# Performance work log

Hardware: AMD Instinct MI355X
Metric: run time of the kernel (lower is better)

## Reference

```python
import jax, jax.numpy as jnp
import numpy as np

C_S, C_Z, C_H, H, PQ, PV = 384, 128, 16, 12, 4, 8
B, N = 1, 512
OUT_DIM = H * (C_H + PV * 4 + C_Z)  # 2112


def setup_inputs() -> dict:
    key = jax.random.key(0)
    ks = jax.random.split(key, 20)
    std = 0.02
    def lin(k, fan_in, fan_out):
        k1, k2 = jax.random.split(k)
        w = jax.random.normal(k1, (fan_in, fan_out), jnp.float32) * std
        b = jax.random.normal(k2, (fan_out,), jnp.float32) * std
        return w, b
    wq, bq = lin(ks[0], C_S, H * C_H)
    wk, bk = lin(ks[1], C_S, H * C_H)
    wv, bv = lin(ks[2], C_S, H * C_H)
    wqp, bqp = lin(ks[3], C_S, H * PQ * 3)
    wkp, bkp = lin(ks[4], C_S, H * PQ * 3)
    wvp, bvp = lin(ks[5], C_S, H * PV * 3)
    wb, bb = lin(ks[6], C_Z, H)
    wo, bo = lin(ks[7], OUT_DIM, C_S)
    return {
        "s": jax.random.normal(ks[8], (B, N, C_S), jnp.float32),
        "z": jax.random.normal(ks[9], (B, N, N, C_Z), jnp.float32),
        "translations": jax.random.normal(ks[10], (B, N, 3), jnp.float32),
        "rotations": jax.random.normal(ks[11], (B, N, 3, 3), jnp.float32),
        "mask": jnp.ones((B, N), jnp.int32),
        "wq": wq, "bq": bq, "wk": wk, "bk": bk, "wv": wv, "bv": bv,
        "wqp": wqp, "bqp": bqp, "wkp": wkp, "bkp": bkp, "wvp": wvp, "bvp": bvp,
        "wb": wb, "bb": bb, "wo": wo, "bo": bo,
    }


def reference(s, z, translations, rotations, mask,
              wq, bq, wk, bk, wv, bv, wqp, bqp, wkp, bkp, wvp, bvp,
              wb, bb, wo, bo):
    b_, n_ = s.shape[0], s.shape[1]
    # scalar q/k/v: (B,N,H,C)
    q = (s @ wq + bq).reshape(b_, n_, H, C_H)
    k = (s @ wk + bk).reshape(b_, n_, H, C_H)
    v = (s @ wv + bv).reshape(b_, n_, H, C_H)
    # points: (B,N,H,P,3), moved to global frame
    qp = (s @ wqp + bqp).reshape(b_, n_, H, PQ, 3)
    kp = (s @ wkp + bkp).reshape(b_, n_, H, PQ, 3)
    t = translations[:, :, None, None, :]  # (B,N,1,1,3)
    qpg = jnp.einsum('bnij,bnhpj->bnhpi', rotations, qp) + t
    kpg = jnp.einsum('bnij,bnhpj->bnhpi', rotations, kp) + t
    # scalar attention: (B,N,M,H)
    attn_scalar = jnp.einsum('bnhc,bmhc->bnmh', q, k) / np.sqrt(C_H).astype(np.float32)
    # point-distance attention: (B,N,M,H)
    diff = qpg[:, :, None] - kpg[:, None]           # (B,N,M,H,P,3)
    attn_points = -0.5 * jnp.sum(diff * diff, axis=(-1, -2))
    # pair bias: (B,N,M,H)
    bias = z @ wb + bb
    attn = attn_scalar + attn_points + bias
    mask2d = (mask[:, None, :] * mask[:, :, None])[..., None]  # (B,N,M,1)
    attn = jnp.where(mask2d == 0, -jnp.inf, attn)
    w = jax.nn.softmax(attn, axis=2)  # over keys M
    # scalar values
    v_out_scalar = jnp.einsum('bnmh,bmhc->bnhc', w, v)
    # point values -> global -> attend -> back to local frame
    vp = (s @ wvp + bvp).reshape(b_, n_, H, PV, 3)
    vpg = jnp.einsum('bnij,bnhpj->bnhpi', rotations, vp) + t
    v_out_points = jnp.einsum('bnmh,bmhpi->bnhpi', w, vpg)
    rot_T = jnp.swapaxes(rotations, -2, -1)
    v_out_points_local = jnp.einsum('bnij,bnhpj->bnhpi', rot_T, v_out_points - t)
    v_out_points_flat = v_out_points_local.reshape(b_, n_, H, PV * 3)
    point_norms = jnp.linalg.norm(v_out_points_local, axis=-1)  # (B,N,H,P)
    # pair features
    pair_features = jnp.einsum('bnmh,bnmc->bnhc', w, z)
    features = jnp.concatenate(
        [v_out_scalar, v_out_points_flat, point_norms, pair_features], axis=-1
    ).reshape(b_, n_, -1)  # (B,N,OUT_DIM)
    return features @ wo + bo
```

## Files before the change

### kernel.cpp

```cpp
#include <hip/hip_runtime.h>

#define NN 512
#define CS 384
#define CZ 128
#define NH 12
#define PROJW 1152
#define FEAT 2112
#define OUTC 384
#define KC 12
#define KTILES 11

#define WPROJ 0
#define WFEAT 589824
#define WW    1671168
#define WOUTP 1671168
#define WKT   4816896

__global__ __launch_bounds__(256) void proj_gemm(
    const float* __restrict__ s,
    const float* __restrict__ wq, const float* __restrict__ bq,
    const float* __restrict__ wk, const float* __restrict__ bk,
    const float* __restrict__ wv, const float* __restrict__ bv,
    const float* __restrict__ wqp, const float* __restrict__ bqp,
    const float* __restrict__ wkp, const float* __restrict__ bkp,
    const float* __restrict__ wvp, const float* __restrict__ bvp,
    const float* __restrict__ rot, const float* __restrict__ trans,
    float* __restrict__ proj, float* __restrict__ kT)
{
    __shared__ float As[32*68];
    __shared__ float Ws[32*52];
    int tid = threadIdx.x;
    int gm0 = blockIdx.x * 64;
    int gc0 = blockIdx.y * 48;
    const float *w, *b; int ldw, lc0;
    if      (gc0 < 192) { w = wq;  b = bq;  ldw = 192; lc0 = gc0;       }
    else if (gc0 < 384) { w = wk;  b = bk;  ldw = 192; lc0 = gc0 - 192; }
    else if (gc0 < 576) { w = wv;  b = bv;  ldw = 192; lc0 = gc0 - 384; }
    else if (gc0 < 720) { w = wqp; b = bqp; ldw = 144; lc0 = gc0 - 576; }
    else if (gc0 < 864) { w = wkp; b = bkp; ldw = 144; lc0 = gc0 - 720; }
    else                { w = wvp; b = bvp; ldw = 288; lc0 = gc0 - 864; }

    int mi = tid >> 4, ni = tid & 15;
    int m0 = mi * 4, n0 = ni * 3;
    float acc[4][3] = {};

    for (int k0 = 0; k0 < CS; k0 += 32) {
        for (int idx = tid; idx < 2048; idx += 256) {
            int r = idx >> 5, c = idx & 31;
            As[c*68 + r] = s[(gm0 + r)*CS + k0 + c];
        }
        for (int idx = tid; idx < 1536; idx += 256) {
            int c = idx / 48, j = idx - c*48;
            Ws[c*52 + j] = w[(k0 + c)*ldw + lc0 + j];
        }
        __syncthreads();
        #pragma unroll 8
        for (int kk = 0; kk < 32; ++kk) {
            float4 a = *(const float4*)&As[kk*68 + m0];
            float w0 = Ws[kk*52 + n0], w1 = Ws[kk*52 + n0 + 1], w2 = Ws[kk*52 + n0 + 2];
            acc[0][0] += a.x*w0; acc[0][1] += a.x*w1; acc[0][2] += a.x*w2;
            acc[1][0] += a.y*w0; acc[1][1] += a.y*w1; acc[1][2] += a.y*w2;
            acc[2][0] += a.z*w0; acc[2][1] += a.z*w1; acc[2][2] += a.z*w2;
            acc[3][0] += a.w*w0; acc[3][1] += a.w*w1; acc[3][2] += a.w*w2;
        }
        __syncthreads();
    }

    float b0 = b[lc0 + n0], b1 = b[lc0 + n0 + 1], b2 = b[lc0 + n0 + 2];
    if (gc0 >= 576) {
        #pragma unroll
        for (int i = 0; i < 4; ++i) {
            int gm = gm0 + m0 + i;
            const float* R = rot + gm*9;
            const float* T = trans + gm*3;
            float x = acc[i][0] + b0, y = acc[i][1] + b1, zz = acc[i][2] + b2;
            float gx = R[0]*x + R[1]*y + R[2]*zz + T[0];
            float gy = R[3]*x + R[4]*y + R[5]*zz + T[1];
            float gz = R[6]*x + R[7]*y + R[8]*zz + T[2];
            float* dst = proj + (size_t)gm*PROJW + gc0 + n0;
            dst[0] = gx; dst[1] = gy; dst[2] = gz;
            if (gc0 >= 720 && gc0 < 864) {
                int c = 192 + (gc0 - 720) + n0;
                kT[(size_t)(c+0)*NN + gm] = gx;
                kT[(size_t)(c+1)*NN + gm] = gy;
                kT[(size_t)(c+2)*NN + gm] = gz;
            }
        }
    } else {
        #pragma unroll
        for (int i = 0; i < 4; ++i) {
            int gm = gm0 + m0 + i;
            float v0 = acc[i][0] + b0, v1 = acc[i][1] + b1, v2 = acc[i][2] + b2;
            float* dst = proj + (size_t)gm*PROJW + gc0 + n0;
            dst[0] = v0; dst[1] = v1; dst[2] = v2;
            if (gc0 >= 192 && gc0 < 384) {
                int c = gc0 - 192 + n0;
                kT[(size_t)(c+0)*NN + gm] = v0;
                kT[(size_t)(c+1)*NN + gm] = v1;
                kT[(size_t)(c+2)*NN + gm] = v2;
            }
        }
    }
}

__global__ __launch_bounds__(256) void bias_gemm(
    const float* __restrict__ z,
    const float* __restrict__ wb, const float* __restrict__ bb,
    float* __restrict__ ww)
{
    __shared__ float zl[64*128];
    __shared__ float sb[64*12];
    int tid = threadIdx.x;
    size_t r0 = (size_t)blockIdx.x * 64;

    const float4* src = (const float4*)(z + r0*CZ);
    float4 v[8];
    #pragma unroll
    for (int k = 0; k < 8; ++k) v[k] = src[tid + k*256];
    #pragma unroll
    for (int k = 0; k < 8; ++k) {
        int i = tid + k*256;
        int r = i >> 5, c4 = i & 31;
        *(float4*)&zl[r*128 + ((c4 ^ (r & 7)) << 2)] = v[k];
    }
    __syncthreads();

    int r = tid & 63, hg = tid >> 6;
    int h0 = __builtin_amdgcn_readfirstlane(hg * 3);
    const float* wbp = wb + h0;
    float a0 = bb[h0], a1 = bb[h0+1], a2 = bb[h0+2];
    #pragma unroll 8
    for (int c4 = 0; c4 < 32; ++c4) {
        float4 zv = *(const float4*)&zl[r*128 + ((c4 ^ (r & 7)) << 2)];
        int cb = c4*4;
        a0 += zv.x*wbp[cb*12]     + zv.y*wbp[(cb+1)*12]     + zv.z*wbp[(cb+2)*12]     + zv.w*wbp[(cb+3)*12];
        a1 += zv.x*wbp[cb*12 + 1] + zv.y*wbp[(cb+1)*12 + 1] + zv.z*wbp[(cb+2)*12 + 1] + zv.w*wbp[(cb+3)*12 + 1];
        a2 += zv.x*wbp[cb*12 + 2] + zv.y*wbp[(cb+1)*12 + 2] + zv.z*wbp[(cb+2)*12 + 2] + zv.w*wbp[(cb+3)*12 + 2];
    }
    float* sd = &sb[r*12 + h0];
    sd[0] = a0; sd[1] = a1; sd[2] = a2;
    __syncthreads();
    if (tid < 192) ((float4*)(ww + r0*12))[tid] = ((const float4*)sb)[tid];
}

__global__ __launch_bounds__(512, 4) void score_kernel(
    const float* __restrict__ proj, const float* __restrict__ kT,
    float* __restrict__ ww,
    const int* __restrict__ mask,
    const float* __restrict__ rot, const float* __restrict__ trans,
    float* __restrict__ feat)
{
    int n = blockIdx.x, tid = threadIdx.x;
    __shared__ float s_e[NN*12];
    __shared__ float s_q[336];
    __shared__ float s_pts[288];
    __shared__ float s_red[384];
    __shared__ float s_M[NH], s_S[NH];

    {
        const float4* src = (const float4*)(ww + (size_t)n*NN*12);
        float4* dst = (float4*)s_e;
        #pragma unroll
        for (int k = 0; k < 3; ++k) dst[tid + k*512] = src[tid + k*512];
    }
    if (tid < 336) s_q[tid] = proj[(size_t)n*PROJW + (tid < 192 ? tid : 384 + tid)];
    int mn = mask[n];
    __syncthreads();

    {
        int m = tid;
        bool ok = (mn != 0) && (mask[m] != 0);
        float sc[12];
        #pragma unroll 2
        for (int h = 0; h < NH; ++h) {
            const float* qh  = &s_q[h*16];
            const float* kTh = kT + (size_t)(h*16)*NN + m;
            float dot = 0.f;
            #pragma unroll
            for (int cc = 0; cc < 16; ++cc) dot += qh[cc] * kTh[(size_t)cc*NN];
            const float* qph  = &s_q[192 + h*12];
            const float* kpTh = kT + (size_t)(192 + h*12)*NN + m;
            float pts = 0.f;
            #pragma unroll
            for (int j = 0; j < 12; ++j) { float d = qph[j] - kpTh[(size_t)j*NN]; pts += d*d; }
            sc[h] = dot*0.25f - 0.5f*pts;
        }
        float* row = &s_e[m*12];
        #pragma unroll
        for (int h = 0; h < NH; ++h) {
            float v = sc[h] + row[h];
            row[h] = ok ? v : -1e30f;
        }
    }
    __syncthreads();
    if (tid < 384) {
        int i = tid / 12, h = tid - i*12;
        float mx = -1e30f;
        for (int mm = i*16; mm < i*16 + 16; ++mm) mx = fmaxf(mx, s_e[mm*12 + h]);
        s_red[tid] = mx;
    }
    __syncthreads();
    if (tid < NH) {
        float mx = -1e30f;
        #pragma unroll
        for (int i = 0; i < 32; ++i) mx = fmaxf(mx, s_red[i*12 + tid]);
        s_M[tid] = mx;
    }
    __syncthreads();
    {
        float M[12];
        #pragma unroll
        for (int h = 0; h < NH; ++h) M[h] = s_M[h];
        float* row = &s_e[tid*12];
        float4 a = *(float4*)row, b4 = *(float4*)(row+4), c4 = *(float4*)(row+8);
        a.x = __expf(a.x - M[0]);  a.y = __expf(a.y - M[1]);
        a.z = __expf(a.z - M[2]);  a.w = __expf(a.w - M[3]);
        b4.x = __expf(b4.x - M[4]); b4.y = __expf(b4.y - M[5]);
        b4.z = __expf(b4.z - M[6]); b4.w = __expf(b4.w - M[7]);
        c4.x = __expf(c4.x - M[8]); c4.y = __expf(c4.y - M[9]);
        c4.z = __expf(c4.z - M[10]); c4.w = __expf(c4.w - M[11]);
        *(float4*)row = a; *(float4*)(row+4) = b4; *(float4*)(row+8) = c4;
    }
    __syncthreads();
    if (tid < 384) {
        int i = tid / 12, h = tid - i*12;
        float sm = 0.f;
        for (int mm = i*16; mm < i*16 + 16; ++mm) sm += s_e[mm*12 + h];
        s_red[tid] = sm;
    }
    __syncthreads();
    if (tid < NH) {
        float sm = 0.f;
        #pragma unroll
        for (int i = 0; i < 32; ++i) sm += s_red[i*12 + tid];
        s_S[tid] = sm;
    }
    __syncthreads();
    {
        float iS[12];
        #pragma unroll
        for (int h = 0; h < NH; ++h) iS[h] = 1.0f / s_S[h];
        float* row = &s_e[tid*12];
        float4 a = *(float4*)row, b4 = *(float4*)(row+4), c4 = *(float4*)(row+8);
        a.x *= iS[0]; a.y *= iS[1]; a.z *= iS[2]; a.w *= iS[3];
        b4.x *= iS[4]; b4.y *= iS[5]; b4.z *= iS[6]; b4.w *= iS[7];
        c4.x *= iS[8]; c4.y *= iS[9]; c4.z *= iS[10]; c4.w *= iS[11];
        *(float4*)row = a; *(float4*)(row+4) = b4; *(float4*)(row+8) = c4;
    }
    __syncthreads();
    {
        float4* dst = (float4*)(ww + (size_t)n*NN*12);
        const float4* src = (const float4*)s_e;
        #pragma unroll
        for (int k = 0; k < 3; ++k) dst[tid + k*512] = src[tid + k*512];
    }

    float* fout = feat + (size_t)n * FEAT;

    {
        int o = tid;
        if (o < 480) {
            int col, h; bool isPt = (o >= 192);
            if (!isPt) { col = 384 + o;       h = o >> 4; }
            else       { int p = o - 192; col = 864 + p; h = p / 24; }
            const float* pc = proj + col;
            float acc0 = 0.f, acc1 = 0.f;
            #pragma unroll 8
            for (int mm = 0; mm < NN; mm += 2) {
                acc0 += s_e[(mm  )*12 + h] * pc[(size_t)(mm  )*PROJW];
                acc1 += s_e[(mm+1)*12 + h] * pc[(size_t)(mm+1)*PROJW];
            }
            float acc = acc0 + acc1;
            if (!isPt) fout[h*176 + (o & 15)] = acc;
            else       s_pts[o - 192] = acc;
        }
    }
    __syncthreads();
    if (tid < 96) {
        int h = tid >> 3, p = tid & 7;
        const float* R = rot + n*9;
        const float* T = trans + n*3;
        float x  = s_pts[h*24 + p*3]     - T[0];
        float y  = s_pts[h*24 + p*3 + 1] - T[1];
        float zz = s_pts[h*24 + p*3 + 2] - T[2];
        float lx = R[0]*x + R[3]*y + R[6]*zz;
        float ly = R[1]*x + R[4]*y + R[7]*zz;
        float lz = R[2]*x + R[5]*y + R[8]*zz;
        float* fo = fout + h*176 + 16;
        fo[p*3] = lx; fo[p*3+1] = ly; fo[p*3+2] = lz;
        fout[h*176 + 40 + p] = sqrtf(lx*lx + ly*ly + lz*lz);
    }
}

__global__ __launch_bounds__(512, 4) void pair_kernel(
    const float* __restrict__ ww, const float* __restrict__ z,
    float* __restrict__ feat)
{
    int n = blockIdx.x, tid = threadIdx.x;
    __shared__ float s_w[NN*12];
    __shared__ float s_p[4*NH*128];
    {
        const float4* src = (const float4*)(ww + (size_t)n*NN*12);
        float4* dst = (float4*)s_w;
        #pragma unroll
        for (int k = 0; k < 3; ++k) dst[tid + k*512] = src[tid + k*512];
    }
    __syncthreads();
    int c = tid & 127, mh = tid >> 7;
    const float* zb = z + ((size_t)n*NN + mh*128) * CZ + c;
    float pacc[12] = {};
    #pragma unroll 4
    for (int mm = 0; mm < 128; ++mm) {
        float zv = zb[(size_t)mm * CZ];
        const float* wr = &s_w[(mh*128 + mm)*12];
        float4 a = *(const float4*)wr, b4 = *(const float4*)(wr+4), c4 = *(const float4*)(wr+8);
        pacc[0] += a.x*zv;  pacc[1] += a.y*zv;  pacc[2] += a.z*zv;  pacc[3] += a.w*zv;
        pacc[4] += b4.x*zv; pacc[5] += b4.y*zv; pacc[6] += b4.z*zv; pacc[7] += b4.w*zv;
        pacc[8] += c4.x*zv; pacc[9] += c4.y*zv; pacc[10] += c4.z*zv; pacc[11] += c4.w*zv;
    }
    #pragma unroll
    for (int h = 0; h < NH; ++h) s_p[(mh*NH + h)*128 + c] = pacc[h];
    __syncthreads();
    {
        float* fout = feat + (size_t)n * FEAT;
        int cc = tid & 127, jh = tid >> 7;
        #pragma unroll
        for (int j = 0; j < 3; ++j) {
            int h = jh*3 + j;
            fout[h*176 + 48 + cc] = s_p[h*128 + cc] + s_p[(NH + h)*128 + cc]
                                  + s_p[(2*NH + h)*128 + cc] + s_p[(3*NH + h)*128 + cc];
        }
    }
}

__global__ __launch_bounds__(256) void out_gemm(
    const float* __restrict__ feat, const float* __restrict__ wo,
    float* __restrict__ pout)
{
    __shared__ float As[16*68];
    __shared__ float Ws[16*68];
    int tid = threadIdx.x;
    int gm0 = blockIdx.x * 64, gn0 = blockIdx.y * 64;
    int kc = blockIdx.z;
    int kbase = kc * (KTILES*16);
    int mi = tid >> 4, ni = tid & 15;
    int m0 = mi * 4, n0 = ni * 4;
    float acc[4][4] = {};

    int ar = tid >> 4, ac = tid & 15;
    int wr = tid >> 6, wc = tid & 63;

    float fa0, fa1, fa2, fa3, wa0, wa1, wa2, wa3;
    float fb0, fb1, fb2, fb3, wb0, wb1, wb2, wb3;
    {
        const float* fp = feat + (size_t)(gm0 + ar)*FEAT + kbase + ac;
        fa0 = fp[0]; fa1 = fp[16*FEAT]; fa2 = fp[32*FEAT]; fa3 = fp[48*FEAT];
        const float* wp = wo + (size_t)(kbase + wr)*OUTC + gn0 + wc;
        wa0 = wp[0]; wa1 = wp[4*OUTC]; wa2 = wp[8*OUTC]; wa3 = wp[12*OUTC];
    }
    for (int kt = 0; kt < KTILES; ++kt) {
        As[ac*68 + ar]      = fa0;
        As[ac*68 + ar + 16] = fa1;
        As[ac*68 + ar + 32] = fa2;
        As[ac*68 + ar + 48] = fa3;
        Ws[wr*68 + wc]        = wa0;
        Ws[(wr+4)*68 + wc]    = wa1;
        Ws[(wr+8)*68 + wc]    = wa2;
        Ws[(wr+12)*68 + wc]   = wa3;
        if (kt + 1 < KTILES) {
            int k0 = kbase + (kt+1)*16;
            const float* fp = feat + (size_t)(gm0 + ar)*FEAT + k0 + ac;
            fb0 = fp[0]; fb1 = fp[16*FEAT]; fb2 = fp[32*FEAT]; fb3 = fp[48*FEAT];
            const float* wp = wo + (size_t)(k0 + wr)*OUTC + gn0 + wc;
            wb0 = wp[0]; wb1 = wp[4*OUTC]; wb2 = wp[8*OUTC]; wb3 = wp[12*OUTC];
        }
        __syncthreads();
        #pragma unroll
        for (int kk = 0; kk < 16; ++kk) {
            float4 a = *(const float4*)&As[kk*68 + m0];
            float4 w = *(const float4*)&Ws[kk*68 + n0];
            acc[0][0] += a.x*w.x; acc[0][1] += a.x*w.y; acc[0][2] += a.x*w.z; acc[0][3] += a.x*w.w;
            acc[1][0] += a.y*w.x; acc[1][1] += a.y*w.y; acc[1][2] += a.y*w.z; acc[1][3] += a.y*w.w;
            acc[2][0] += a.z*w.x; acc[2][1] += a.z*w.y; acc[2][2] += a.z*w.z; acc[2][3] += a.z*w.w;
            acc[3][0] += a.w*w.x; acc[3][1] += a.w*w.y; acc[3][2] += a.w*w.z; acc[3][3] += a.w*w.w;
        }
        __syncthreads();
        fa0 = fb0; fa1 = fb1; fa2 = fb2; fa3 = fb3;
        wa0 = wb0; wa1 = wb1; wa2 = wb2; wa3 = wb3;
    }
    float* pb = pout + (size_t)kc * (NN*OUTC);
    #pragma unroll
    for (int i = 0; i < 4; ++i)
        *(float4*)&pb[(size_t)(gm0 + m0 + i)*OUTC + gn0 + n0] =
            make_float4(acc[i][0], acc[i][1], acc[i][2], acc[i][3]);
}

__global__ __launch_bounds__(256) void out_reduce(
    const float* __restrict__ pout, const float* __restrict__ bo,
    float* __restrict__ out)
{
    int idx4 = blockIdx.x * 256 + threadIdx.x;
    int col4 = idx4 % 96;
    const float4* b4 = (const float4*)bo;
    float4 acc = b4[col4];
    #pragma unroll
    for (int kc = 0; kc < KC; ++kc) {
        float4 p = ((const float4*)(pout + (size_t)kc*(NN*OUTC)))[idx4];
        acc.x += p.x; acc.y += p.y; acc.z += p.z; acc.w += p.w;
    }
    ((float4*)out)[idx4] = acc;
}

extern "C" void kernel_launch(void* const* d_in, const int* in_sizes, int n_in,
                              void* d_out, int out_size, void* d_ws, size_t ws_size,
                              hipStream_t stream) {
    (void)in_sizes; (void)n_in; (void)out_size; (void)ws_size;
    const float* s     = (const float*)d_in[0];
    const float* z     = (const float*)d_in[1];
    const float* trans = (const float*)d_in[2];
    const float* rot   = (const float*)d_in[3];
    const int*   mask  = (const int*)d_in[4];
    const float* wq    = (const float*)d_in[5];
    const float* bq    = (const float*)d_in[6];
    const float* wk    = (const float*)d_in[7];
    const float* bk    = (const float*)d_in[8];
    const float* wv    = (const float*)d_in[9];
    const float* bv    = (const float*)d_in[10];
    const float* wqp   = (const float*)d_in[11];
    const float* bqp   = (const float*)d_in[12];
    const float* wkp   = (const float*)d_in[13];
    const float* bkp   = (const float*)d_in[14];
    const float* wvp   = (const float*)d_in[15];
    const float* bvp   = (const float*)d_in[16];
    const float* wb    = (const float*)d_in[17];
    const float* bb    = (const float*)d_in[18];
    const float* wo    = (const float*)d_in[19];
    const float* bo    = (const float*)d_in[20];
    float* ws  = (float*)d_ws;
    float* out = (float*)d_out;

    bias_gemm<<<4096, 256, 0, stream>>>(z, wb, bb, ws + WW);
    proj_gemm<<<dim3(8, 24), 256, 0, stream>>>(
        s, wq, bq, wk, bk, wv, bv, wqp, bqp, wkp, bkp, wvp, bvp, rot, trans,
        ws + WPROJ, ws + WKT);
    score_kernel<<<NN, 512, 0, stream>>>(ws + WPROJ, ws + WKT, ws + WW, mask, rot, trans, ws + WFEAT);
    pair_kernel<<<NN, 512, 0, stream>>>(ws + WW, z, ws + WFEAT);
    out_gemm<<<dim3(8, 6, KC), 256, 0, stream>>>(ws + WFEAT, wo, ws + WOUTP);
    out_reduce<<<192, 256, 0, stream>>>(ws + WOUTP, bo, out);
}
```

Before: 386.8 us.

## Merge bias and projection GEMMs into one launch, atomically reduce split-K output

The pair-bias GEMM, the projection GEMM and an output bias-initialisation step now run as branches of a single launch selected by block index. The output GEMM's split-K partials go straight into the output with float atomics, and the K split goes from 12 to 33 chunks, so the separate reduce kernel and its partial buffer are gone. This cuts launch count and workspace traffic, at the cost of many more atomics, a result whose rounding depends on summation order, and a larger unified shared memory footprint for the fused kernel.

```diff
diff --git a/kernel.cpp b/kernel.cpp
--- a/kernel.cpp
+++ b/kernel.cpp
@@ -7,16 +7,15 @@
 #define PROJW 1152
 #define FEAT 2112
 #define OUTC 384
-#define KC 12
-#define KTILES 11
+#define KC 33
+#define KTILES 4
 
 #define WPROJ 0
 #define WFEAT 589824
 #define WW    1671168
-#define WOUTP 1671168
 #define WKT   4816896
 
-__global__ __launch_bounds__(256) void proj_gemm(
+__global__ __launch_bounds__(256) void fused_pre(
     const float* __restrict__ s,
     const float* __restrict__ wq, const float* __restrict__ bq,
     const float* __restrict__ wk, const float* __restrict__ bk,
@@ -25,13 +24,60 @@
     const float* __restrict__ wkp, const float* __restrict__ bkp,
     const float* __restrict__ wvp, const float* __restrict__ bvp,
     const float* __restrict__ rot, const float* __restrict__ trans,
-    float* __restrict__ proj, float* __restrict__ kT)
+    const float* __restrict__ z,
+    const float* __restrict__ wb, const float* __restrict__ bb,
+    const float* __restrict__ bo,
+    float* __restrict__ proj, float* __restrict__ kT,
+    float* __restrict__ ww, float* __restrict__ out)
 {
-    __shared__ float As[32*68];
-    __shared__ float Ws[32*52];
-    int tid = threadIdx.x;
-    int gm0 = blockIdx.x * 64;
-    int gc0 = blockIdx.y * 48;
+    __shared__ float smem[8960];
+    int bx = blockIdx.x, tid = threadIdx.x;
+
+    if (bx >= 4288) {
+        int idx4 = (bx - 4288)*256 + tid;
+        ((float4*)out)[idx4] = ((const float4*)bo)[idx4 % 96];
+        return;
+    }
+
+    if (bx < 4096) {
+        float* zl = smem;
+        float* sb = smem + 8192;
+        size_t r0 = (size_t)bx * 64;
+        const float4* src = (const float4*)(z + r0*CZ);
+        float4 v[8];
+        #pragma unroll
+        for (int k = 0; k < 8; ++k) v[k] = src[tid + k*256];
+        #pragma unroll
+        for (int k = 0; k < 8; ++k) {
+            int i = tid + k*256;
+            int r = i >> 5, c4 = i & 31;
+            *(float4*)&zl[r*128 + ((c4 ^ (r & 7)) << 2)] = v[k];
+        }
+        __syncthreads();
+        int r = tid & 63, hg = tid >> 6;
+        int h0 = __builtin_amdgcn_readfirstlane(hg * 3);
+        const float* wbp = wb + h0;
+        float a0 = bb[h0], a1 = bb[h0+1], a2 = bb[h0+2];
+        #pragma unroll 8
+        for (int c4 = 0; c4 < 32; ++c4) {
+            float4 zv = *(const float4*)&zl[r*128 + ((c4 ^ (r & 7)) << 2)];
+            int cb = c4*4;
+            a0 += zv.x*wbp[cb*12]     + zv.y*wbp[(cb+1)*12]     + zv.z*wbp[(cb+2)*12]     + zv.w*wbp[(cb+3)*12];
+            a1 += zv.x*wbp[cb*12 + 1] + zv.y*wbp[(cb+1)*12 + 1] + zv.z*wbp[(cb+2)*12 + 1] + zv.w*wbp[(cb+3)*12 + 1];
+            a2 += zv.x*wbp[cb*12 + 2] + zv.y*wbp[(cb+1)*12 + 2] + zv.z*wbp[(cb+2)*12 + 2] + zv.w*wbp[(cb+3)*12 + 2];
+        }
+        float* sd = &sb[r*12 + h0];
+        sd[0] = a0; sd[1] = a1; sd[2] = a2;
+        __syncthreads();
+        if (tid < 192) ((float4*)(ww + r0*12))[tid] = ((const float4*)sb)[tid];
+        return;
+    }
+
+    float* As = smem;
+    float* Ws = smem + 2176;
+    int p = bx - 4096;
+    int gm0 = (p & 7) * 64;
+    int gc0 = (p >> 3) * 48;
     const float *w, *b; int ldw, lc0;
     if      (gc0 < 192) { w = wq;  b = bq;  ldw = 192; lc0 = gc0;       }
     else if (gc0 < 384) { w = wk;  b = bk;  ldw = 192; lc0 = gc0 - 192; }
@@ -103,46 +149,6 @@
     }
 }
 
-__global__ __launch_bounds__(256) void bias_gemm(
-    const float* __restrict__ z,
-    const float* __restrict__ wb, const float* __restrict__ bb,
-    float* __restrict__ ww)
-{
-    __shared__ float zl[64*128];
-    __shared__ float sb[64*12];
-    int tid = threadIdx.x;
-    size_t r0 = (size_t)blockIdx.x * 64;
-
-    const float4* src = (const float4*)(z + r0*CZ);
-    float4 v[8];
-    #pragma unroll
-    for (int k = 0; k < 8; ++k) v[k] = src[tid + k*256];
-    #pragma unroll
-    for (int k = 0; k < 8; ++k) {
-        int i = tid + k*256;
-        int r = i >> 5, c4 = i & 31;
-        *(float4*)&zl[r*128 + ((c4 ^ (r & 7)) << 2)] = v[k];
-    }
-    __syncthreads();
-
-    int r = tid & 63, hg = tid >> 6;
-    int h0 = __builtin_amdgcn_readfirstlane(hg * 3);
-    const float* wbp = wb + h0;
-    float a0 = bb[h0], a1 = bb[h0+1], a2 = bb[h0+2];
-    #pragma unroll 8
-    for (int c4 = 0; c4 < 32; ++c4) {
-        float4 zv = *(const float4*)&zl[r*128 + ((c4 ^ (r & 7)) << 2)];
-        int cb = c4*4;
-        a0 += zv.x*wbp[cb*12]     + zv.y*wbp[(cb+1)*12]     + zv.z*wbp[(cb+2)*12]     + zv.w*wbp[(cb+3)*12];
-        a1 += zv.x*wbp[cb*12 + 1] + zv.y*wbp[(cb+1)*12 + 1] + zv.z*wbp[(cb+2)*12 + 1] + zv.w*wbp[(cb+3)*12 + 1];
-        a2 += zv.x*wbp[cb*12 + 2] + zv.y*wbp[(cb+1)*12 + 2] + zv.z*wbp[(cb+2)*12 + 2] + zv.w*wbp[(cb+3)*12 + 2];
-    }
-    float* sd = &sb[r*12 + h0];
-    sd[0] = a0; sd[1] = a1; sd[2] = a2;
-    __syncthreads();
-    if (tid < 192) ((float4*)(ww + r0*12))[tid] = ((const float4*)sb)[tid];
-}
-
 __global__ __launch_bounds__(512, 4) void score_kernel(
     const float* __restrict__ proj, const float* __restrict__ kT,
     float* __restrict__ ww,
@@ -335,7 +341,7 @@
 
 __global__ __launch_bounds__(256) void out_gemm(
     const float* __restrict__ feat, const float* __restrict__ wo,
-    float* __restrict__ pout)
+    float* __restrict__ out)
 {
     __shared__ float As[16*68];
     __shared__ float Ws[16*68];
@@ -388,27 +394,14 @@
         fa0 = fb0; fa1 = fb1; fa2 = fb2; fa3 = fb3;
         wa0 = wb0; wa1 = wb1; wa2 = wb2; wa3 = wb3;
     }
-    float* pb = pout + (size_t)kc * (NN*OUTC);
     #pragma unroll
-    for (int i = 0; i < 4; ++i)
-        *(float4*)&pb[(size_t)(gm0 + m0 + i)*OUTC + gn0 + n0] =
-            make_float4(acc[i][0], acc[i][1], acc[i][2], acc[i][3]);
-}
-
-__global__ __launch_bounds__(256) void out_reduce(
-    const float* __restrict__ pout, const float* __restrict__ bo,
-    float* __restrict__ out)
-{
-    int idx4 = blockIdx.x * 256 + threadIdx.x;
-    int col4 = idx4 % 96;
-    const float4* b4 = (const float4*)bo;
-    float4 acc = b4[col4];
-    #pragma unroll
-    for (int kc = 0; kc < KC; ++kc) {
-        float4 p = ((const float4*)(pout + (size_t)kc*(NN*OUTC)))[idx4];
-        acc.x += p.x; acc.y += p.y; acc.z += p.z; acc.w += p.w;
-    }
-    ((float4*)out)[idx4] = acc;
+    for (int i = 0; i < 4; ++i) {
+        float* op = &out[(size_t)(gm0 + m0 + i)*OUTC + gn0 + n0];
+        unsafeAtomicAdd(op + 0, acc[i][0]);
+        unsafeAtomicAdd(op + 1, acc[i][1]);
+        unsafeAtomicAdd(op + 2, acc[i][2]);
+        unsafeAtomicAdd(op + 3, acc[i][3]);
+    }
 }
 
 extern "C" void kernel_launch(void* const* d_in, const int* in_sizes, int n_in,
@@ -439,12 +432,10 @@
     float* ws  = (float*)d_ws;
     float* out = (float*)d_out;
 
-    bias_gemm<<<4096, 256, 0, stream>>>(z, wb, bb, ws + WW);
-    proj_gemm<<<dim3(8, 24), 256, 0, stream>>>(
+    fused_pre<<<4480, 256, 0, stream>>>(
         s, wq, bq, wk, bk, wv, bv, wqp, bqp, wkp, bkp, wvp, bvp, rot, trans,
-        ws + WPROJ, ws + WKT);
+        z, wb, bb, bo, ws + WPROJ, ws + WKT, ws + WW, out);
     score_kernel<<<NN, 512, 0, stream>>>(ws + WPROJ, ws + WKT, ws + WW, mask, rot, trans, ws + WFEAT);
     pair_kernel<<<NN, 512, 0, stream>>>(ws + WW, z, ws + WFEAT);
-    out_gemm<<<dim3(8, 6, KC), 256, 0, stream>>>(ws + WFEAT, wo, ws + WOUTP);
-    out_reduce<<<192, 256, 0, stream>>>(ws + WOUTP, bo, out);
+    out_gemm<<<dim3(8, 6, KC), 256, 0, stream>>>(ws + WFEAT, wo, out);
 }
```

Measured after the change: 449.8 us. 1.16x slower.

## Double threads per block in score and pair kernels, splitting heads and keys

Applied to the files above, without the earlier changes.

Raises score_kernel and pair_kernel from 512 to 1024 threads per block. Each thread now handles 6 heads instead of 12, and the value aggregation splits the key range in two with a shared-memory combine step. The aim is more parallelism and latency hiding per block, since only 512 blocks run on the device. The cost is an extra barrier, extra shared memory, and possible register pressure or lower occupancy from the 1024-thread launch bound. bias_gemm is moved in the file but not changed.

```diff
diff --git a/kernel.cpp b/kernel.cpp
--- a/kernel.cpp
+++ b/kernel.cpp
@@ -15,6 +15,46 @@
 #define WW    1671168
 #define WOUTP 1671168
 #define WKT   4816896
+
+__global__ __launch_bounds__(256) void bias_gemm(
+    const float* __restrict__ z,
+    const float* __restrict__ wb, const float* __restrict__ bb,
+    float* __restrict__ ww)
+{
+    __shared__ float zl[64*128];
+    __shared__ float sb[64*12];
+    int tid = threadIdx.x;
+    size_t r0 = (size_t)blockIdx.x * 64;
+
+    const float4* src = (const float4*)(z + r0*CZ);
+    float4 v[8];
+    #pragma unroll
+    for (int k = 0; k < 8; ++k) v[k] = src[tid + k*256];
+    #pragma unroll
+    for (int k = 0; k < 8; ++k) {
+        int i = tid + k*256;
+        int r = i >> 5, c4 = i & 31;
+        *(float4*)&zl[r*128 + ((c4 ^ (r & 7)) << 2)] = v[k];
+    }
+    __syncthreads();
+
+    int r = tid & 63, hg = tid >> 6;
+    int h0 = __builtin_amdgcn_readfirstlane(hg * 3);
+    const float* wbp = wb + h0;
+    float a0 = bb[h0], a1 = bb[h0+1], a2 = bb[h0+2];
+    #pragma unroll 8
+    for (int c4 = 0; c4 < 32; ++c4) {
+        float4 zv = *(const float4*)&zl[r*128 + ((c4 ^ (r & 7)) << 2)];
+        int cb = c4*4;
+        a0 += zv.x*wbp[cb*12]     + zv.y*wbp[(cb+1)*12]     + zv.z*wbp[(cb+2)*12]     + zv.w*wbp[(cb+3)*12];
+        a1 += zv.x*wbp[cb*12 + 1] + zv.y*wbp[(cb+1)*12 + 1] + zv.z*wbp[(cb+2)*12 + 1] + zv.w*wbp[(cb+3)*12 + 1];
+        a2 += zv.x*wbp[cb*12 + 2] + zv.y*wbp[(cb+1)*12 + 2] + zv.z*wbp[(cb+2)*12 + 2] + zv.w*wbp[(cb+3)*12 + 2];
+    }
+    float* sd = &sb[r*12 + h0];
+    sd[0] = a0; sd[1] = a1; sd[2] = a2;
+    __syncthreads();
+    if (tid < 192) ((float4*)(ww + r0*12))[tid] = ((const float4*)sb)[tid];
+}
 
 __global__ __launch_bounds__(256) void proj_gemm(
     const float* __restrict__ s,
@@ -103,47 +143,7 @@
     }
 }
 
-__global__ __launch_bounds__(256) void bias_gemm(
-    const float* __restrict__ z,
-    const float* __restrict__ wb, const float* __restrict__ bb,
-    float* __restrict__ ww)
-{
-    __shared__ float zl[64*128];
-    __shared__ float sb[64*12];
-    int tid = threadIdx.x;
-    size_t r0 = (size_t)blockIdx.x * 64;
-
-    const float4* src = (const float4*)(z + r0*CZ);
-    float4 v[8];
-    #pragma unroll
-    for (int k = 0; k < 8; ++k) v[k] = src[tid + k*256];
-    #pragma unroll
-    for (int k = 0; k < 8; ++k) {
-        int i = tid + k*256;
-        int r = i >> 5, c4 = i & 31;
-        *(float4*)&zl[r*128 + ((c4 ^ (r & 7)) << 2)] = v[k];
-    }
-    __syncthreads();
-
-    int r = tid & 63, hg = tid >> 6;
-    int h0 = __builtin_amdgcn_readfirstlane(hg * 3);
-    const float* wbp = wb + h0;
-    float a0 = bb[h0], a1 = bb[h0+1], a2 = bb[h0+2];
-    #pragma unroll 8
-    for (int c4 = 0; c4 < 32; ++c4) {
-        float4 zv = *(const float4*)&zl[r*128 + ((c4 ^ (r & 7)) << 2)];
-        int cb = c4*4;
-        a0 += zv.x*wbp[cb*12]     + zv.y*wbp[(cb+1)*12]     + zv.z*wbp[(cb+2)*12]     + zv.w*wbp[(cb+3)*12];
-        a1 += zv.x*wbp[cb*12 + 1] + zv.y*wbp[(cb+1)*12 + 1] + zv.z*wbp[(cb+2)*12 + 1] + zv.w*wbp[(cb+3)*12 + 1];
-        a2 += zv.x*wbp[cb*12 + 2] + zv.y*wbp[(cb+1)*12 + 2] + zv.z*wbp[(cb+2)*12 + 2] + zv.w*wbp[(cb+3)*12 + 2];
-    }
-    float* sd = &sb[r*12 + h0];
-    sd[0] = a0; sd[1] = a1; sd[2] = a2;
-    __syncthreads();
-    if (tid < 192) ((float4*)(ww + r0*12))[tid] = ((const float4*)sb)[tid];
-}
-
-__global__ __launch_bounds__(512, 4) void score_kernel(
+__global__ __launch_bounds__(1024, 4) void score_kernel(
     const float* __restrict__ proj, const float* __restrict__ kT,
     float* __restrict__ ww,
     const int* __restrict__ mask,
@@ -153,26 +153,28 @@
     int n = blockIdx.x, tid = threadIdx.x;
     __shared__ float s_e[NN*12];
     __shared__ float s_q[336];
+    __shared__ float s_acc[2*480];
     __shared__ float s_pts[288];
-    __shared__ float s_red[384];
+    __shared__ float s_red[768];
     __shared__ float s_M[NH], s_S[NH];
 
     {
         const float4* src = (const float4*)(ww + (size_t)n*NN*12);
         float4* dst = (float4*)s_e;
-        #pragma unroll
-        for (int k = 0; k < 3; ++k) dst[tid + k*512] = src[tid + k*512];
+        dst[tid] = src[tid];
+        if (tid < 512) dst[tid + 1024] = src[tid + 1024];
     }
     if (tid < 336) s_q[tid] = proj[(size_t)n*PROJW + (tid < 192 ? tid : 384 + tid)];
     int mn = mask[n];
     __syncthreads();
 
     {
-        int m = tid;
+        int m = tid & 511, h0 = (tid >> 9) * 6;
         bool ok = (mn != 0) && (mask[m] != 0);
-        float sc[12];
-        #pragma unroll 2
-        for (int h = 0; h < NH; ++h) {
+        float sc[6];
+        #pragma unroll
+        for (int j = 0; j < 6; ++j) {
+            int h = h0 + j;
             const float* qh  = &s_q[h*16];
             const float* kTh = kT + (size_t)(h*16)*NN + m;
             float dot = 0.f;
@@ -182,98 +184,92 @@
             const float* kpTh = kT + (size_t)(192 + h*12)*NN + m;
             float pts = 0.f;
             #pragma unroll
-            for (int j = 0; j < 12; ++j) { float d = qph[j] - kpTh[(size_t)j*NN]; pts += d*d; }
-            sc[h] = dot*0.25f - 0.5f*pts;
-        }
-        float* row = &s_e[m*12];
-        #pragma unroll
-        for (int h = 0; h < NH; ++h) {
-            float v = sc[h] + row[h];
-            row[h] = ok ? v : -1e30f;
-        }
-    }
-    __syncthreads();
-    if (tid < 384) {
+            for (int jj = 0; jj < 12; ++jj) { float d = qph[jj] - kpTh[(size_t)jj*NN]; pts += d*d; }
+            sc[j] = dot*0.25f - 0.5f*pts;
+        }
+        float* row = &s_e[m*12 + h0];
+        #pragma unroll
+        for (int j = 0; j < 6; ++j) {
+            float v = sc[j] + row[j];
+            row[j] = ok ? v : -1e30f;
+        }
+    }
+    __syncthreads();
+    if (tid < 768) {
         int i = tid / 12, h = tid - i*12;
         float mx = -1e30f;
-        for (int mm = i*16; mm < i*16 + 16; ++mm) mx = fmaxf(mx, s_e[mm*12 + h]);
+        for (int mm = i*8; mm < i*8 + 8; ++mm) mx = fmaxf(mx, s_e[mm*12 + h]);
         s_red[tid] = mx;
     }
     __syncthreads();
     if (tid < NH) {
         float mx = -1e30f;
         #pragma unroll
-        for (int i = 0; i < 32; ++i) mx = fmaxf(mx, s_red[i*12 + tid]);
+        for (int i = 0; i < 64; ++i) mx = fmaxf(mx, s_red[i*12 + tid]);
         s_M[tid] = mx;
     }
     __syncthreads();
     {
-        float M[12];
-        #pragma unroll
-        for (int h = 0; h < NH; ++h) M[h] = s_M[h];
-        float* row = &s_e[tid*12];
-        float4 a = *(float4*)row, b4 = *(float4*)(row+4), c4 = *(float4*)(row+8);
-        a.x = __expf(a.x - M[0]);  a.y = __expf(a.y - M[1]);
-        a.z = __expf(a.z - M[2]);  a.w = __expf(a.w - M[3]);
-        b4.x = __expf(b4.x - M[4]); b4.y = __expf(b4.y - M[5]);
-        b4.z = __expf(b4.z - M[6]); b4.w = __expf(b4.w - M[7]);
-        c4.x = __expf(c4.x - M[8]); c4.y = __expf(c4.y - M[9]);
-        c4.z = __expf(c4.z - M[10]); c4.w = __expf(c4.w - M[11]);
-        *(float4*)row = a; *(float4*)(row+4) = b4; *(float4*)(row+8) = c4;
-    }
-    __syncthreads();
-    if (tid < 384) {
+        int m = tid & 511, h0 = (tid >> 9) * 6;
+        float* row = &s_e[m*12 + h0];
+        #pragma unroll
+        for (int j = 0; j < 6; ++j) row[j] = __expf(row[j] - s_M[h0 + j]);
+    }
+    __syncthreads();
+    if (tid < 768) {
         int i = tid / 12, h = tid - i*12;
         float sm = 0.f;
-        for (int mm = i*16; mm < i*16 + 16; ++mm) sm += s_e[mm*12 + h];
+        for (int mm = i*8; mm < i*8 + 8; ++mm) sm += s_e[mm*12 + h];
         s_red[tid] = sm;
     }
     __syncthreads();
     if (tid < NH) {
         float sm = 0.f;
         #pragma unroll
-        for (int i = 0; i < 32; ++i) sm += s_red[i*12 + tid];
+        for (int i = 0; i < 64; ++i) sm += s_red[i*12 + tid];
         s_S[tid] = sm;
     }
     __syncthreads();
     {
-        float iS[12];
-        #pragma unroll
-        for (int h = 0; h < NH; ++h) iS[h] = 1.0f / s_S[h];
-        float* row = &s_e[tid*12];
-        float4 a = *(float4*)row, b4 = *(float4*)(row+4), c4 = *(float4*)(row+8);
-        a.x *= iS[0]; a.y *= iS[1]; a.z *= iS[2]; a.w *= iS[3];
-        b4.x *= iS[4]; b4.y *= iS[5]; b4.z *= iS[6]; b4.w *= iS[7];
-        c4.x *= iS[8]; c4.y *= iS[9]; c4.z *= iS[10]; c4.w *= iS[11];
-        *(float4*)row = a; *(float4*)(row+4) = b4; *(float4*)(row+8) = c4;
+        int m = tid & 511, h0 = (tid >> 9) * 6;
+        float* row = &s_e[m*12 + h0];
+        float i0 = 1.0f / s_S[h0], i1 = 1.0f / s_S[h0+1], i2 = 1.0f / s_S[h0+2];
+        float i3 = 1.0f / s_S[h0+3], i4 = 1.0f / s_S[h0+4], i5 = 1.0f / s_S[h0+5];
+        row[0] *= i0; row[1] *= i1; row[2] *= i2;
+        row[3] *= i3; row[4] *= i4; row[5] *= i5;
     }
     __syncthreads();
     {
         float4* dst = (float4*)(ww + (size_t)n*NN*12);
         const float4* src = (const float4*)s_e;
-        #pragma unroll
-        for (int k = 0; k < 3; ++k) dst[tid + k*512] = src[tid + k*512];
+        dst[tid] = src[tid];
+        if (tid < 512) dst[tid + 1024] = src[tid + 1024];
     }
 
     float* fout = feat + (size_t)n * FEAT;
 
     {
-        int o = tid;
+        int o = tid & 511, seg = tid >> 9;
         if (o < 480) {
             int col, h; bool isPt = (o >= 192);
             if (!isPt) { col = 384 + o;       h = o >> 4; }
             else       { int p = o - 192; col = 864 + p; h = p / 24; }
             const float* pc = proj + col;
+            int mbeg = seg * 256;
             float acc0 = 0.f, acc1 = 0.f;
             #pragma unroll 8
-            for (int mm = 0; mm < NN; mm += 2) {
+            for (int mm = mbeg; mm < mbeg + 256; mm += 2) {
                 acc0 += s_e[(mm  )*12 + h] * pc[(size_t)(mm  )*PROJW];
                 acc1 += s_e[(mm+1)*12 + h] * pc[(size_t)(mm+1)*PROJW];
             }
-            float acc = acc0 + acc1;
-            if (!isPt) fout[h*176 + (o & 15)] = acc;
-            else       s_pts[o - 192] = acc;
-        }
+            s_acc[seg*480 + o] = acc0 + acc1;
+        }
+    }
+    __syncthreads();
+    if (tid < 480) {
+        float acc = s_acc[tid] + s_acc[480 + tid];
+        if (tid < 192) { int h = tid >> 4; fout[h*176 + (tid & 15)] = acc; }
+        else           { s_pts[tid - 192] = acc; }
     }
     __syncthreads();
     if (tid < 96) {
@@ -292,7 +288,7 @@
     }
 }
 
-__global__ __launch_bounds__(512, 4) void pair_kernel(
+__global__ __launch_bounds__(1024, 4) void pair_kernel(
     const float* __restrict__ ww, const float* __restrict__ z,
     float* __restrict__ feat)
 {
@@ -302,31 +298,29 @@
     {
         const float4* src = (const float4*)(ww + (size_t)n*NN*12);
         float4* dst = (float4*)s_w;
-        #pragma unroll
-        for (int k = 0; k < 3; ++k) dst[tid + k*512] = src[tid + k*512];
-    }
-    __syncthreads();
-    int c = tid & 127, mh = tid >> 7;
+        dst[tid] = src[tid];
+        if (tid < 512) dst[tid + 1024] = src[tid + 1024];
+    }
+    __syncthreads();
+    int c = tid & 127;
+    int mh = (tid >> 7) & 3;
+    int h0 = (tid >> 9) * 6;
     const float* zb = z + ((size_t)n*NN + mh*128) * CZ + c;
-    float pacc[12] = {};
+    float pacc[6] = {};
     #pragma unroll 4
     for (int mm = 0; mm < 128; ++mm) {
         float zv = zb[(size_t)mm * CZ];
-        const float* wr = &s_w[(mh*128 + mm)*12];
-        float4 a = *(const float4*)wr, b4 = *(const float4*)(wr+4), c4 = *(const float4*)(wr+8);
-        pacc[0] += a.x*zv;  pacc[1] += a.y*zv;  pacc[2] += a.z*zv;  pacc[3] += a.w*zv;
-        pacc[4] += b4.x*zv; pacc[5] += b4.y*zv; pacc[6] += b4.z*zv; pacc[7] += b4.w*zv;
-        pacc[8] += c4.x*zv; pacc[9] += c4.y*zv; pacc[10] += c4.z*zv; pacc[11] += c4.w*zv;
+        const float* wr = &s_w[(mh*128 + mm)*12 + h0];
+        pacc[0] += wr[0]*zv; pacc[1] += wr[1]*zv; pacc[2] += wr[2]*zv;
+        pacc[3] += wr[3]*zv; pacc[4] += wr[4]*zv; pacc[5] += wr[5]*zv;
     }
     #pragma unroll
-    for (int h = 0; h < NH; ++h) s_p[(mh*NH + h)*128 + c] = pacc[h];
+    for (int j = 0; j < 6; ++j) s_p[(mh*NH + h0 + j)*128 + c] = pacc[j];
     __syncthreads();
     {
         float* fout = feat + (size_t)n * FEAT;
-        int cc = tid & 127, jh = tid >> 7;
-        #pragma unroll
-        for (int j = 0; j < 3; ++j) {
-            int h = jh*3 + j;
+        for (int idx = tid; idx < 1536; idx += 1024) {
+            int h = idx >> 7, cc = idx & 127;
             fout[h*176 + 48 + cc] = s_p[h*128 + cc] + s_p[(NH + h)*128 + cc]
                                   + s_p[(2*NH + h)*128 + cc] + s_p[(3*NH + h)*128 + cc];
         }
@@ -443,8 +437,8 @@
     proj_gemm<<<dim3(8, 24), 256, 0, stream>>>(
         s, wq, bq, wk, bk, wv, bv, wqp, bqp, wkp, bkp, wvp, bvp, rot, trans,
         ws + WPROJ, ws + WKT);
-    score_kernel<<<NN, 512, 0, stream>>>(ws + WPROJ, ws + WKT, ws + WW, mask, rot, trans, ws + WFEAT);
-    pair_kernel<<<NN, 512, 0, stream>>>(ws + WW, z, ws + WFEAT);
+    score_kernel<<<NN, 1024, 0, stream>>>(ws + WPROJ, ws + WKT, ws + WW, mask, rot, trans, ws + WFEAT);
+    pair_kernel<<<NN, 1024, 0, stream>>>(ws + WW, z, ws + WFEAT);
     out_gemm<<<dim3(8, 6, KC), 256, 0, stream>>>(ws + WFEAT, wo, ws + WOUTP);
     out_reduce<<<192, 256, 0, stream>>>(ws + WOUTP, bo, out);
 }
```

After: 402.9 us. +4.2%, slower.
